# Performance work log

Measured on AMD Instinct MI355X. Metric: run time of the kernel, lower is better.

Reference implementation:

```python
import jax, jax.numpy as jnp
import numpy as np

B, N, CIN = 8, 16384, 256
G, K, C, H, L = 16, 128, 256, 8, 2


def setup_inputs() -> dict:
    key = jax.random.key(0)
    ks = jax.random.split(key, 8)
    f = lambda k, s: jax.random.normal(k, s, dtype=jnp.float32)
    return dict(
        x=f(ks[0], (B, N, CIN)),
        W_lin=f(ks[1], (CIN, C)) * 0.02,
        b_lin=jnp.zeros((C,), jnp.float32),
        emb=f(ks[2], (G, K, C)),  # learned_embedding ~ randn in torch
        in_proj_w=f(ks[3], (L, 3 * C, C)) * 0.02,
        in_proj_b=jnp.zeros((L, 3 * C), jnp.float32),
        out_w=f(ks[4], (L, C, C)) * 0.02,
        out_b=jnp.zeros((L, C), jnp.float32),
        lin_w=f(ks[5], (L, C, C)) * 0.02,
        lin_b=jnp.zeros((L, C), jnp.float32),
        ln1_w=jnp.ones((L, C), jnp.float32),
        ln1_b=jnp.zeros((L, C), jnp.float32),
        ln2_w=jnp.ones((L, C), jnp.float32),
        ln2_b=jnp.zeros((L, C), jnp.float32),
    )


def _layernorm(x, w, b, eps=1e-5):
    m = x.mean(-1, keepdims=True)
    v = jnp.var(x, axis=-1, keepdims=True)
    return (x - m) / jnp.sqrt(v + eps) * w + b


def reference(x, W_lin, b_lin, emb, in_proj_w, in_proj_b, out_w, out_b,
              lin_w, lin_b, ln1_w, ln1_b, ln2_w, ln2_b):
    B_, N_, Cin = x.shape
    T = N_ // G  # tokens per group
    # grouped projection: [B,G,T,C]
    x4 = x.reshape(B_, G, T, Cin) @ W_lin + b_lin
    # cross-attn scores [B,G,K,T]; softmax over the LATENT axis k (dim=-2)
    scores = jnp.einsum('gkd,bgtd->bgkt', emb, x4) * (1.0 / jnp.sqrt(jnp.float32(C)))
    attn = jax.nn.softmax(scores, axis=2)
    y = jnp.einsum('bgkt,bgtd->bgkd', attn, x4)  # [B,G,K,C]
    # torch MHA with batch_first=False: (B*G) is SEQUENCE, K is BATCH
    y = y.reshape(B_ * G, K, C)  # (S, Nb, C)
    S = B_ * G
    Dh = C // H
    scale = 1.0 / jnp.sqrt(jnp.float32(Dh))
    for i in range(L):
        qkv = y @ in_proj_w[i].T + in_proj_b[i]
        q, k, v = jnp.split(qkv, 3, axis=-1)
        q = q.reshape(S, K, H, Dh)
        k = k.reshape(S, K, H, Dh)
        v = v.reshape(S, K, H, Dh)
        s2 = jnp.einsum('snhd,tnhd->nhst', q, k) * scale  # (Nb,H,S,S)
        a = jax.nn.softmax(s2, axis=-1)
        o = jnp.einsum('nhst,tnhd->snhd', a, v).reshape(S, K, C)
        o = o @ out_w[i].T + out_b[i]
        y = _layernorm(o + y, ln1_w[i], ln1_b[i])
        y = _layernorm(y @ lin_w[i].T + lin_b[i] + y, ln2_w[i], ln2_b[i])
    out = y.reshape(B_, G * K, C)
    return (out, attn)
```

## Files before the change

kernel.cpp:

```cpp
#include <hip/hip_runtime.h>

typedef __attribute__((ext_vector_type(4))) float  f32x4;
typedef __attribute__((ext_vector_type(8))) short  s16x8;

static __device__ __forceinline__ short f2bf(float f) {
    unsigned int x = __builtin_bit_cast(unsigned int, f);
    x += 0x7fffu + ((x >> 16) & 1u);
    return (short)(x >> 16);
}

__global__ __launch_bounds__(256) void castk(const float* __restrict__ in,
                                             short* __restrict__ out, int n) {
    int i = blockIdx.x * 256 + threadIdx.x;
    if (i < n) out[i] = f2bf(in[i]);
}

__global__ __launch_bounds__(256) void tcast256(const float* __restrict__ in,
                                                short* __restrict__ out) {
    out[blockIdx.x * 256 + threadIdx.x] = f2bf(in[threadIdx.x * 256 + blockIdx.x]);
}

template<bool AF32, bool OF32, bool OB16>
__global__ __launch_bounds__(256) void gemm_bt(
    const void* __restrict__ Av, const short* __restrict__ Bm,
    const float* __restrict__ bias,
    float* __restrict__ Cf, short* __restrict__ Cb,
    int M, int N, int K)
{
    __shared__ short lsA[128 * 40];
    __shared__ short lsB[128 * 40];
    const int tid = threadIdx.x;
    const int m0 = blockIdx.x * 128;
    const int n0 = blockIdx.y * 128;
    const int lane = tid & 63;
    const int w = tid >> 6;
    const int wmi = w >> 1, wni = w & 1;
    const int lr = lane & 15, ko = lane >> 4;
    const int r0 = tid >> 1, oc0 = (tid * 2) & 3;

    f32x4 acc[4][4] = {};
    for (int k0 = 0; k0 < K; k0 += 32) {
        __syncthreads();
        if constexpr (AF32) {
            const float* Ap = (const float*)Av + (size_t)(m0 + r0) * K + k0 + oc0 * 8;
            f32x4 a0 = *(const f32x4*)(Ap);
            f32x4 a1 = *(const f32x4*)(Ap + 4);
            f32x4 a2 = *(const f32x4*)(Ap + 8);
            f32x4 a3 = *(const f32x4*)(Ap + 12);
            s16x8 w0, w1;
            #pragma unroll
            for (int j = 0; j < 4; ++j) {
                w0[j] = f2bf(a0[j]); w0[4 + j] = f2bf(a1[j]);
                w1[j] = f2bf(a2[j]); w1[4 + j] = f2bf(a3[j]);
            }
            *(s16x8*)&lsA[r0 * 40 + oc0 * 8]     = w0;
            *(s16x8*)&lsA[r0 * 40 + oc0 * 8 + 8] = w1;
        } else {
            const short* Ap = (const short*)Av + (size_t)(m0 + r0) * K + k0 + oc0 * 8;
            *(s16x8*)&lsA[r0 * 40 + oc0 * 8]     = *(const s16x8*)Ap;
            *(s16x8*)&lsA[r0 * 40 + oc0 * 8 + 8] = *(const s16x8*)(Ap + 8);
        }
        const short* Bp = Bm + (size_t)(n0 + r0) * K + k0 + oc0 * 8;
        *(s16x8*)&lsB[r0 * 40 + oc0 * 8]     = *(const s16x8*)Bp;
        *(s16x8*)&lsB[r0 * 40 + oc0 * 8 + 8] = *(const s16x8*)(Bp + 8);
        __syncthreads();
        #pragma unroll
        for (int mt = 0; mt < 4; ++mt) {
            s16x8 a = *(const s16x8*)&lsA[(wmi * 64 + mt * 16 + lr) * 40 + ko * 8];
            #pragma unroll
            for (int nt = 0; nt < 4; ++nt) {
                s16x8 b = *(const s16x8*)&lsB[(wni * 64 + nt * 16 + lr) * 40 + ko * 8];
                acc[mt][nt] = __builtin_amdgcn_mfma_f32_16x16x32_bf16(a, b, acc[mt][nt], 0, 0, 0);
            }
        }
    }
    const int cr = ko * 4, cc = lr;
    #pragma unroll
    for (int mt = 0; mt < 4; ++mt)
    #pragma unroll
    for (int nt = 0; nt < 4; ++nt) {
        const int col = n0 + wni * 64 + nt * 16 + cc;
        const float bv = bias ? bias[col] : 0.f;
        #pragma unroll
        for (int j = 0; j < 4; ++j) {
            const int row = m0 + wmi * 64 + mt * 16 + cr + j;
            float v = acc[mt][nt][j] + bv;
            size_t idx = (size_t)row * N + col;
            if constexpr (OF32) Cf[idx] = v;
            if constexpr (OB16) Cb[idx] = f2bf(v);
        }
    }
}

__global__ __launch_bounds__(256) void scores_softmax(
    const short* __restrict__ embb, const short* __restrict__ x4b,
    float* __restrict__ attnF, short* __restrict__ attnB)
{
    __shared__ short lsA[128 * 40];
    __shared__ short lsB[128 * 40];
    __shared__ float redm[2 * 128];
    __shared__ float reds[2 * 128];
    const int tid = threadIdx.x;
    const int z = blockIdx.y;
    const int g = z & 15;
    const int t0 = blockIdx.x * 128;
    const short* A = embb + (size_t)g * 32768;
    const short* B = x4b + (size_t)z * 262144 + (size_t)t0 * 256;
    const int lane = tid & 63;
    const int w = tid >> 6;
    const int wmi = w >> 1, wni = w & 1;
    const int lr = lane & 15, ko = lane >> 4;
    const int r0 = tid >> 1, oc0 = (tid * 2) & 3;

    f32x4 acc[4][4] = {};
    for (int k0 = 0; k0 < 256; k0 += 32) {
        __syncthreads();
        const short* Ap = A + (size_t)r0 * 256 + k0 + oc0 * 8;
        *(s16x8*)&lsA[r0 * 40 + oc0 * 8]     = *(const s16x8*)Ap;
        *(s16x8*)&lsA[r0 * 40 + oc0 * 8 + 8] = *(const s16x8*)(Ap + 8);
        const short* Bp = B + (size_t)r0 * 256 + k0 + oc0 * 8;
        *(s16x8*)&lsB[r0 * 40 + oc0 * 8]     = *(const s16x8*)Bp;
        *(s16x8*)&lsB[r0 * 40 + oc0 * 8 + 8] = *(const s16x8*)(Bp + 8);
        __syncthreads();
        #pragma unroll
        for (int mt = 0; mt < 4; ++mt) {
            s16x8 a = *(const s16x8*)&lsA[(wmi * 64 + mt * 16 + lr) * 40 + ko * 8];
            #pragma unroll
            for (int nt = 0; nt < 4; ++nt) {
                s16x8 b = *(const s16x8*)&lsB[(wni * 64 + nt * 16 + lr) * 40 + ko * 8];
                acc[mt][nt] = __builtin_amdgcn_mfma_f32_16x16x32_bf16(a, b, acc[mt][nt], 0, 0, 0);
            }
        }
    }
    const float scale = 0.0625f;
    float cm[4];
    #pragma unroll
    for (int nt = 0; nt < 4; ++nt) {
        float m = -1e30f;
        #pragma unroll
        for (int mt = 0; mt < 4; ++mt)
            #pragma unroll
            for (int j = 0; j < 4; ++j) m = fmaxf(m, acc[mt][nt][j]);
        m = fmaxf(m, __shfl_xor(m, 16));
        m = fmaxf(m, __shfl_xor(m, 32));
        cm[nt] = m * scale;
    }
    if (lane < 16) {
        #pragma unroll
        for (int nt = 0; nt < 4; ++nt)
            redm[wmi * 128 + wni * 64 + nt * 16 + lr] = cm[nt];
    }
    __syncthreads();
    float cmax[4];
    #pragma unroll
    for (int nt = 0; nt < 4; ++nt) {
        int c = wni * 64 + nt * 16 + lr;
        cmax[nt] = fmaxf(redm[c], redm[128 + c]);
    }
    float cs[4];
    #pragma unroll
    for (int nt = 0; nt < 4; ++nt) {
        float s = 0.f;
        #pragma unroll
        for (int mt = 0; mt < 4; ++mt)
            #pragma unroll
            for (int j = 0; j < 4; ++j) {
                float p = __expf(acc[mt][nt][j] * scale - cmax[nt]);
                acc[mt][nt][j] = p;
                s += p;
            }
        s += __shfl_xor(s, 16);
        s += __shfl_xor(s, 32);
        cs[nt] = s;
    }
    if (lane < 16) {
        #pragma unroll
        for (int nt = 0; nt < 4; ++nt)
            reds[wmi * 128 + wni * 64 + nt * 16 + lr] = cs[nt];
    }
    __syncthreads();
    #pragma unroll
    for (int nt = 0; nt < 4; ++nt) {
        int c = wni * 64 + nt * 16 + lr;
        float inv = 1.f / (reds[c] + reds[128 + c]);
        int col = t0 + c;
        #pragma unroll
        for (int mt = 0; mt < 4; ++mt)
            #pragma unroll
            for (int j = 0; j < 4; ++j) {
                int row = wmi * 64 + mt * 16 + ko * 4 + j;
                float a = acc[mt][nt][j] * inv;
                size_t idx = ((size_t)(z * 128 + row)) * 1024 + col;
                attnF[idx] = a;
                attnB[idx] = f2bf(a);
            }
    }
}

__global__ __launch_bounds__(256) void y_gemm(
    const short* __restrict__ attnB, const short* __restrict__ x4b,
    float* __restrict__ yF, short* __restrict__ yB)
{
    __shared__ short lsA[128 * 40];
    __shared__ short lsB[128 * 40];
    const int tid = threadIdx.x;
    const int z = blockIdx.y;
    const int d0 = blockIdx.x * 128;
    const short* A = attnB + (size_t)z * 131072;
    const short* X = x4b + (size_t)z * 262144 + d0;
    const int lane = tid & 63;
    const int w = tid >> 6;
    const int wmi = w >> 1, wni = w & 1;
    const int lr = lane & 15, ko = lane >> 4;
    const int r0 = tid >> 1, oc0 = (tid * 2) & 3;
    const int rb = tid >> 3, ocb = (tid * 2) & 15;
    f32x4 acc[4][4] = {};
    for (int k0 = 0; k0 < 1024; k0 += 32) {
        __syncthreads();
        const short* Ap = A + (size_t)r0 * 1024 + k0 + oc0 * 8;
        *(s16x8*)&lsA[r0 * 40 + oc0 * 8]     = *(const s16x8*)Ap;
        *(s16x8*)&lsA[r0 * 40 + oc0 * 8 + 8] = *(const s16x8*)(Ap + 8);
        s16x8 v0 = *(const s16x8*)(X + (size_t)(k0 + rb) * 256 + ocb * 8);
        s16x8 v1 = *(const s16x8*)(X + (size_t)(k0 + rb) * 256 + ocb * 8 + 8);
        #pragma unroll
        for (int j = 0; j < 8; ++j) {
            int dd = ocb * 8 + j;
            lsB[dd * 40 + ((((rb >> 3) ^ ((dd >> 4) & 3)) << 3) | (rb & 7))] = v0[j];
            int dd2 = dd + 8;
            lsB[dd2 * 40 + ((((rb >> 3) ^ ((dd2 >> 4) & 3)) << 3) | (rb & 7))] = v1[j];
        }
        __syncthreads();
        #pragma unroll
        for (int mt = 0; mt < 4; ++mt) {
            s16x8 a = *(const s16x8*)&lsA[(wmi * 64 + mt * 16 + lr) * 40 + ko * 8];
            #pragma unroll
            for (int nt = 0; nt < 4; ++nt) {
                int dd = wni * 64 + nt * 16 + lr;
                s16x8 b = *(const s16x8*)&lsB[dd * 40 + ((ko ^ ((dd >> 4) & 3)) << 3)];
                acc[mt][nt] = __builtin_amdgcn_mfma_f32_16x16x32_bf16(a, b, acc[mt][nt], 0, 0, 0);
            }
        }
    }
    const int cr = ko * 4, cc = lr;
    #pragma unroll
    for (int mt = 0; mt < 4; ++mt)
    #pragma unroll
    for (int nt = 0; nt < 4; ++nt)
        #pragma unroll
        for (int j = 0; j < 4; ++j) {
            int krow = wmi * 64 + mt * 16 + cr + j;
            int col = d0 + wni * 64 + nt * 16 + cc;
            float v = acc[mt][nt][j];
            size_t idx = ((size_t)(z * 128 + krow)) * 256 + col;
            yF[idx] = v;
            yB[idx] = f2bf(v);
        }
}

__global__ __launch_bounds__(256) void mha(
    const short* __restrict__ qkvb, short* __restrict__ ob)
{
    __shared__ short la[128 * 136];
    __shared__ short lvt[32 * 136];
    __shared__ float redm[2 * 128];
    __shared__ float reds[2 * 128];
    short* lq = la;
    short* lk = la + 128 * 40;
    const int tid = threadIdx.x;
    const int nb = blockIdx.x >> 3;
    const int h = blockIdx.x & 7;
    const int lane = tid & 63;
    const int w = tid >> 6;
    const int wmi = w >> 1, wni = w & 1;
    const int lr = lane & 15, ko = lane >> 4;
    const int sv = tid >> 1, oc0 = (tid * 2) & 3;
    {
        const short* qp = qkvb + ((size_t)sv * 128 + nb) * 768 + h * 32 + oc0 * 8;
        *(s16x8*)&lq[sv * 40 + oc0 * 8]     = *(const s16x8*)qp;
        *(s16x8*)&lq[sv * 40 + oc0 * 8 + 8] = *(const s16x8*)(qp + 8);
        const short* kp = qp + 256;
        *(s16x8*)&lk[sv * 40 + oc0 * 8]     = *(const s16x8*)kp;
        *(s16x8*)&lk[sv * 40 + oc0 * 8 + 8] = *(const s16x8*)(kp + 8);
        const short* vp = qp + 512;
        s16x8 v0 = *(const s16x8*)vp;
        s16x8 v1 = *(const s16x8*)(vp + 8);
        #pragma unroll
        for (int j = 0; j < 8; ++j) {
            lvt[(oc0 * 8 + j) * 136 + sv]     = v0[j];
            lvt[(oc0 * 8 + 8 + j) * 136 + sv] = v1[j];
        }
    }
    __syncthreads();
    f32x4 acc[4][4] = {};
    #pragma unroll
    for (int mt = 0; mt < 4; ++mt) {
        s16x8 a = *(const s16x8*)&lq[(wmi * 64 + mt * 16 + lr) * 40 + ko * 8];
        #pragma unroll
        for (int nt = 0; nt < 4; ++nt) {
            s16x8 b = *(const s16x8*)&lk[(wni * 64 + nt * 16 + lr) * 40 + ko * 8];
            acc[mt][nt] = __builtin_amdgcn_mfma_f32_16x16x32_bf16(a, b, acc[mt][nt], 0, 0, 0);
        }
    }
    const float scale = 0.1767766953f;
    float rm[4][4];
    #pragma unroll
    for (int mt = 0; mt < 4; ++mt)
        #pragma unroll
        for (int j = 0; j < 4; ++j) {
            float m = -1e30f;
            #pragma unroll
            for (int nt = 0; nt < 4; ++nt) m = fmaxf(m, acc[mt][nt][j]);
            m = fmaxf(m, __shfl_xor(m, 1));
            m = fmaxf(m, __shfl_xor(m, 2));
            m = fmaxf(m, __shfl_xor(m, 4));
            m = fmaxf(m, __shfl_xor(m, 8));
            rm[mt][j] = m * scale;
        }
    if (lr == 0) {
        #pragma unroll
        for (int mt = 0; mt < 4; ++mt)
            #pragma unroll
            for (int j = 0; j < 4; ++j)
                redm[wni * 128 + wmi * 64 + mt * 16 + ko * 4 + j] = rm[mt][j];
    }
    __syncthreads();
    float rs[4][4];
    #pragma unroll
    for (int mt = 0; mt < 4; ++mt)
        #pragma unroll
        for (int j = 0; j < 4; ++j) {
            int row = wmi * 64 + mt * 16 + ko * 4 + j;
            float mx = fmaxf(redm[row], redm[128 + row]);
            float s = 0.f;
            #pragma unroll
            for (int nt = 0; nt < 4; ++nt) {
                float p = __expf(acc[mt][nt][j] * scale - mx);
                acc[mt][nt][j] = p;
                s += p;
            }
            s += __shfl_xor(s, 1);
            s += __shfl_xor(s, 2);
            s += __shfl_xor(s, 4);
            s += __shfl_xor(s, 8);
            rs[mt][j] = s;
        }
    if (lr == 0) {
        #pragma unroll
        for (int mt = 0; mt < 4; ++mt)
            #pragma unroll
            for (int j = 0; j < 4; ++j)
                reds[wni * 128 + wmi * 64 + mt * 16 + ko * 4 + j] = rs[mt][j];
    }
    __syncthreads();
    #pragma unroll
    for (int mt = 0; mt < 4; ++mt)
        #pragma unroll
        for (int j = 0; j < 4; ++j) {
            int row = wmi * 64 + mt * 16 + ko * 4 + j;
            float inv = 1.f / (reds[row] + reds[128 + row]);
            #pragma unroll
            for (int nt = 0; nt < 4; ++nt) {
                int col = wni * 64 + nt * 16 + lr;
                la[row * 136 + col] = f2bf(acc[mt][nt][j] * inv);
            }
        }
    __syncthreads();
    f32x4 acc2[2][2] = {};
    #pragma unroll
    for (int ks = 0; ks < 4; ++ks)
        #pragma unroll
        for (int mt = 0; mt < 2; ++mt) {
            s16x8 a = *(const s16x8*)&la[(w * 32 + mt * 16 + lr) * 136 + ks * 32 + ko * 8];
            #pragma unroll
            for (int nt = 0; nt < 2; ++nt) {
                s16x8 b = *(const s16x8*)&lvt[(nt * 16 + lr) * 136 + ks * 32 + ko * 8];
                acc2[mt][nt] = __builtin_amdgcn_mfma_f32_16x16x32_bf16(a, b, acc2[mt][nt], 0, 0, 0);
            }
        }
    const int cr = ko * 4, cc = lr;
    #pragma unroll
    for (int mt = 0; mt < 2; ++mt)
    #pragma unroll
    for (int nt = 0; nt < 2; ++nt)
        #pragma unroll
        for (int j = 0; j < 4; ++j) {
            int s = w * 32 + mt * 16 + cr + j;
            int d = nt * 16 + cc;
            ob[((size_t)s * 128 + nb) * 256 + h * 32 + d] = f2bf(acc2[mt][nt][j]);
        }
}

__global__ __launch_bounds__(256) void ln_res(
    const float* __restrict__ zin, const float* __restrict__ res,
    const float* __restrict__ gw, const float* __restrict__ gb,
    float* __restrict__ outF, short* __restrict__ outB)
{
    const int row = blockIdx.x;
    const int t = threadIdx.x;
    const size_t idx = (size_t)row * 256 + t;
    float v = zin[idx] + res[idx];
    float s1 = v, s2 = v * v;
    #pragma unroll
    for (int o = 1; o < 64; o <<= 1) {
        s1 += __shfl_xor(s1, o);
        s2 += __shfl_xor(s2, o);
    }
    __shared__ float ps[8];
    const int wv = t >> 6;
    if ((t & 63) == 0) { ps[wv] = s1; ps[4 + wv] = s2; }
    __syncthreads();
    float S1 = ps[0] + ps[1] + ps[2] + ps[3];
    float S2 = ps[4] + ps[5] + ps[6] + ps[7];
    float m = S1 * 0.00390625f;
    float var = S2 * 0.00390625f - m * m;
    float rstd = rsqrtf(var + 1e-5f);
    float o = (v - m) * rstd * gw[t] + gb[t];
    outF[idx] = o;
    outB[idx] = f2bf(o);
}

extern "C" void kernel_launch(void* const* d_in, const int* in_sizes, int n_in,
                              void* d_out, int out_size, void* d_ws, size_t ws_size,
                              hipStream_t stream)
{
    const float* x    = (const float*)d_in[0];
    const float* Wlin = (const float*)d_in[1];
    const float* blin = (const float*)d_in[2];
    const float* emb  = (const float*)d_in[3];
    const float* ipw  = (const float*)d_in[4];
    const float* ipb  = (const float*)d_in[5];
    const float* outw = (const float*)d_in[6];
    const float* outb = (const float*)d_in[7];
    const float* linw = (const float*)d_in[8];
    const float* linb = (const float*)d_in[9];
    const float* ln1w = (const float*)d_in[10];
    const float* ln1b = (const float*)d_in[11];
    const float* ln2w = (const float*)d_in[12];
    const float* ln2b = (const float*)d_in[13];

    char* ws = (char*)d_ws;
    short* x4_b   = (short*)(ws);
    short* attn_b = (short*)(ws + 67108864);
    float* yF     = (float*)(ws + 100663296);
    short* y_b    = (short*)(ws + 117440512);
    char*  wb     = ws + 125829120;
    short* WT_b   = (short*)(wb);
    short* emb_b  = (short*)(wb + 131072);
    short* inw_b  = (short*)(wb + 131072 + 1048576);
    short* outw_b = (short*)(wb + 131072 + 1048576 + 786432);
    short* linw_b = (short*)(wb + 131072 + 1048576 + 786432 + 262144);
    short* qkv_b  = (short*)(ws);
    short* o_b    = (short*)(ws + 25165824);
    float* op     = (float*)(ws + 33554432);

    float* out_y    = (float*)d_out;
    float* out_attn = (float*)d_out + 4194304;

    castk<<<dim3(2048), dim3(256), 0, stream>>>(emb, emb_b, 524288);
    castk<<<dim3(1536), dim3(256), 0, stream>>>(ipw, inw_b, 393216);
    castk<<<dim3(512),  dim3(256), 0, stream>>>(outw, outw_b, 131072);
    castk<<<dim3(512),  dim3(256), 0, stream>>>(linw, linw_b, 131072);
    tcast256<<<dim3(256), dim3(256), 0, stream>>>(Wlin, WT_b);

    gemm_bt<true, false, true><<<dim3(1024, 2), dim3(256), 0, stream>>>(
        x, WT_b, blin, nullptr, x4_b, 131072, 256, 256);
    scores_softmax<<<dim3(8, 128), dim3(256), 0, stream>>>(emb_b, x4_b, out_attn, attn_b);
    y_gemm<<<dim3(2, 128), dim3(256), 0, stream>>>(attn_b, x4_b, yF, y_b);

    for (int i = 0; i < 2; ++i) {
        gemm_bt<false, false, true><<<dim3(128, 6), dim3(256), 0, stream>>>(
            y_b, inw_b + i * 196608, ipb + i * 768, nullptr, qkv_b, 16384, 768, 256);
        mha<<<dim3(1024), dim3(256), 0, stream>>>(qkv_b, o_b);
        gemm_bt<false, true, false><<<dim3(128, 2), dim3(256), 0, stream>>>(
            o_b, outw_b + i * 65536, outb + i * 256, op, nullptr, 16384, 256, 256);
        ln_res<<<dim3(16384), dim3(256), 0, stream>>>(
            op, yF, ln1w + i * 256, ln1b + i * 256, yF, y_b);
        gemm_bt<false, true, false><<<dim3(128, 2), dim3(256), 0, stream>>>(
            y_b, linw_b + i * 65536, linb + i * 256, op, nullptr, 16384, 256, 256);
        ln_res<<<dim3(16384), dim3(256), 0, stream>>>(
            op, yF, ln2w + i * 256, ln2b + i * 256, (i == 1) ? out_y : yF, y_b);
    }
}
```

Before: 561.9 us.

## Prefetch next K-tile into registers in GEMM kernels and merge weight casts

The GEMM-style kernels (gemm_bt, scores_softmax, y_gemm) now issue the global loads for the next K-slice into registers before running the MFMA loop on the current LDS tile. This lets global memory latency overlap with compute instead of stalling at the top of each iteration. The four separate weight-cast launches are merged into one vectorized castall kernel, which cuts launch overhead. The prefetch adds register pressure, and the barrier count per iteration stays at two.

```diff
diff --git a/kernel.cpp b/kernel.cpp
--- a/kernel.cpp
+++ b/kernel.cpp
@@ -2,6 +2,7 @@
 
 typedef __attribute__((ext_vector_type(4))) float  f32x4;
 typedef __attribute__((ext_vector_type(8))) short  s16x8;
+typedef __attribute__((ext_vector_type(4))) short  s16x4;
 
 static __device__ __forceinline__ short f2bf(float f) {
     unsigned int x = __builtin_bit_cast(unsigned int, f);
@@ -9,10 +10,23 @@
     return (short)(x >> 16);
 }
 
-__global__ __launch_bounds__(256) void castk(const float* __restrict__ in,
-                                             short* __restrict__ out, int n) {
-    int i = blockIdx.x * 256 + threadIdx.x;
-    if (i < n) out[i] = f2bf(in[i]);
+__global__ __launch_bounds__(256) void castall(
+    const float* __restrict__ emb, const float* __restrict__ ipw,
+    const float* __restrict__ outw, const float* __restrict__ linw,
+    short* __restrict__ de, short* __restrict__ di,
+    short* __restrict__ dg, short* __restrict__ dl)
+{
+    int q = blockIdx.x * 256 + threadIdx.x;
+    const float* s; short* d; int o;
+    if (q < 131072)      { s = emb;  d = de; o = q; }
+    else if (q < 229376) { s = ipw;  d = di; o = q - 131072; }
+    else if (q < 262144) { s = outw; d = dg; o = q - 229376; }
+    else                 { s = linw; d = dl; o = q - 262144; }
+    f32x4 v = *(const f32x4*)(s + (size_t)o * 4);
+    s16x4 r;
+    #pragma unroll
+    for (int j = 0; j < 4; ++j) r[j] = f2bf(v[j]);
+    *(s16x4*)(d + (size_t)o * 4) = r;
 }
 
 __global__ __launch_bounds__(256) void tcast256(const float* __restrict__ in,
@@ -38,32 +52,56 @@
     const int lr = lane & 15, ko = lane >> 4;
     const int r0 = tid >> 1, oc0 = (tid * 2) & 3;
 
+    const float* Apf = (const float*)Av + (size_t)(m0 + r0) * K + oc0 * 8;
+    const short* Aps = (const short*)Av + (size_t)(m0 + r0) * K + oc0 * 8;
+    const short* Bp  = Bm + (size_t)(n0 + r0) * K + oc0 * 8;
+
+    f32x4 pa0, pa1, pa2, pa3;
+    s16x8 pas0, pas1, pb0, pb1;
+    if constexpr (AF32) {
+        pa0 = *(const f32x4*)(Apf);
+        pa1 = *(const f32x4*)(Apf + 4);
+        pa2 = *(const f32x4*)(Apf + 8);
+        pa3 = *(const f32x4*)(Apf + 12);
+    } else {
+        pas0 = *(const s16x8*)(Aps);
+        pas1 = *(const s16x8*)(Aps + 8);
+    }
+    pb0 = *(const s16x8*)(Bp);
+    pb1 = *(const s16x8*)(Bp + 8);
+
     f32x4 acc[4][4] = {};
     for (int k0 = 0; k0 < K; k0 += 32) {
-        __syncthreads();
         if constexpr (AF32) {
-            const float* Ap = (const float*)Av + (size_t)(m0 + r0) * K + k0 + oc0 * 8;
-            f32x4 a0 = *(const f32x4*)(Ap);
-            f32x4 a1 = *(const f32x4*)(Ap + 4);
-            f32x4 a2 = *(const f32x4*)(Ap + 8);
-            f32x4 a3 = *(const f32x4*)(Ap + 12);
             s16x8 w0, w1;
             #pragma unroll
             for (int j = 0; j < 4; ++j) {
-                w0[j] = f2bf(a0[j]); w0[4 + j] = f2bf(a1[j]);
-                w1[j] = f2bf(a2[j]); w1[4 + j] = f2bf(a3[j]);
+                w0[j] = f2bf(pa0[j]); w0[4 + j] = f2bf(pa1[j]);
+                w1[j] = f2bf(pa2[j]); w1[4 + j] = f2bf(pa3[j]);
             }
             *(s16x8*)&lsA[r0 * 40 + oc0 * 8]     = w0;
             *(s16x8*)&lsA[r0 * 40 + oc0 * 8 + 8] = w1;
         } else {
-            const short* Ap = (const short*)Av + (size_t)(m0 + r0) * K + k0 + oc0 * 8;
-            *(s16x8*)&lsA[r0 * 40 + oc0 * 8]     = *(const s16x8*)Ap;
-            *(s16x8*)&lsA[r0 * 40 + oc0 * 8 + 8] = *(const s16x8*)(Ap + 8);
-        }
-        const short* Bp = Bm + (size_t)(n0 + r0) * K + k0 + oc0 * 8;
-        *(s16x8*)&lsB[r0 * 40 + oc0 * 8]     = *(const s16x8*)Bp;
-        *(s16x8*)&lsB[r0 * 40 + oc0 * 8 + 8] = *(const s16x8*)(Bp + 8);
+            *(s16x8*)&lsA[r0 * 40 + oc0 * 8]     = pas0;
+            *(s16x8*)&lsA[r0 * 40 + oc0 * 8 + 8] = pas1;
+        }
+        *(s16x8*)&lsB[r0 * 40 + oc0 * 8]     = pb0;
+        *(s16x8*)&lsB[r0 * 40 + oc0 * 8 + 8] = pb1;
         __syncthreads();
+        if (k0 + 32 < K) {
+            const int kn = k0 + 32;
+            if constexpr (AF32) {
+                pa0 = *(const f32x4*)(Apf + kn);
+                pa1 = *(const f32x4*)(Apf + kn + 4);
+                pa2 = *(const f32x4*)(Apf + kn + 8);
+                pa3 = *(const f32x4*)(Apf + kn + 12);
+            } else {
+                pas0 = *(const s16x8*)(Aps + kn);
+                pas1 = *(const s16x8*)(Aps + kn + 8);
+            }
+            pb0 = *(const s16x8*)(Bp + kn);
+            pb1 = *(const s16x8*)(Bp + kn + 8);
+        }
         #pragma unroll
         for (int mt = 0; mt < 4; ++mt) {
             s16x8 a = *(const s16x8*)&lsA[(wmi * 64 + mt * 16 + lr) * 40 + ko * 8];
@@ -73,6 +111,7 @@
                 acc[mt][nt] = __builtin_amdgcn_mfma_f32_16x16x32_bf16(a, b, acc[mt][nt], 0, 0, 0);
             }
         }
+        __syncthreads();
     }
     const int cr = ko * 4, cc = lr;
     #pragma unroll
@@ -112,16 +151,27 @@
     const int lr = lane & 15, ko = lane >> 4;
     const int r0 = tid >> 1, oc0 = (tid * 2) & 3;
 
+    const short* Ap = A + (size_t)r0 * 256 + oc0 * 8;
+    const short* Bp = B + (size_t)r0 * 256 + oc0 * 8;
+    s16x8 pa0 = *(const s16x8*)(Ap);
+    s16x8 pa1 = *(const s16x8*)(Ap + 8);
+    s16x8 pb0 = *(const s16x8*)(Bp);
+    s16x8 pb1 = *(const s16x8*)(Bp + 8);
+
     f32x4 acc[4][4] = {};
     for (int k0 = 0; k0 < 256; k0 += 32) {
+        *(s16x8*)&lsA[r0 * 40 + oc0 * 8]     = pa0;
+        *(s16x8*)&lsA[r0 * 40 + oc0 * 8 + 8] = pa1;
+        *(s16x8*)&lsB[r0 * 40 + oc0 * 8]     = pb0;
+        *(s16x8*)&lsB[r0 * 40 + oc0 * 8 + 8] = pb1;
         __syncthreads();
-        const short* Ap = A + (size_t)r0 * 256 + k0 + oc0 * 8;
-        *(s16x8*)&lsA[r0 * 40 + oc0 * 8]     = *(const s16x8*)Ap;
-        *(s16x8*)&lsA[r0 * 40 + oc0 * 8 + 8] = *(const s16x8*)(Ap + 8);
-        const short* Bp = B + (size_t)r0 * 256 + k0 + oc0 * 8;
-        *(s16x8*)&lsB[r0 * 40 + oc0 * 8]     = *(const s16x8*)Bp;
-        *(s16x8*)&lsB[r0 * 40 + oc0 * 8 + 8] = *(const s16x8*)(Bp + 8);
-        __syncthreads();
+        if (k0 + 32 < 256) {
+            const int kn = k0 + 32;
+            pa0 = *(const s16x8*)(Ap + kn);
+            pa1 = *(const s16x8*)(Ap + kn + 8);
+            pb0 = *(const s16x8*)(Bp + kn);
+            pb1 = *(const s16x8*)(Bp + kn + 8);
+        }
         #pragma unroll
         for (int mt = 0; mt < 4; ++mt) {
             s16x8 a = *(const s16x8*)&lsA[(wmi * 64 + mt * 16 + lr) * 40 + ko * 8];
@@ -131,6 +181,7 @@
                 acc[mt][nt] = __builtin_amdgcn_mfma_f32_16x16x32_bf16(a, b, acc[mt][nt], 0, 0, 0);
             }
         }
+        __syncthreads();
     }
     const float scale = 0.0625f;
     float cm[4];
@@ -214,22 +265,33 @@
     const int lr = lane & 15, ko = lane >> 4;
     const int r0 = tid >> 1, oc0 = (tid * 2) & 3;
     const int rb = tid >> 3, ocb = (tid * 2) & 15;
+
+    const short* Ap = A + (size_t)r0 * 1024 + oc0 * 8;
+    const short* Xp = X + (size_t)rb * 256 + ocb * 8;
+
+    s16x8 pa0 = *(const s16x8*)(Ap);
+    s16x8 pa1 = *(const s16x8*)(Ap + 8);
+    s16x8 pv0 = *(const s16x8*)(Xp);
+    s16x8 pv1 = *(const s16x8*)(Xp + 8);
+
     f32x4 acc[4][4] = {};
     for (int k0 = 0; k0 < 1024; k0 += 32) {
-        __syncthreads();
-        const short* Ap = A + (size_t)r0 * 1024 + k0 + oc0 * 8;
-        *(s16x8*)&lsA[r0 * 40 + oc0 * 8]     = *(const s16x8*)Ap;
-        *(s16x8*)&lsA[r0 * 40 + oc0 * 8 + 8] = *(const s16x8*)(Ap + 8);
-        s16x8 v0 = *(const s16x8*)(X + (size_t)(k0 + rb) * 256 + ocb * 8);
-        s16x8 v1 = *(const s16x8*)(X + (size_t)(k0 + rb) * 256 + ocb * 8 + 8);
+        *(s16x8*)&lsA[r0 * 40 + oc0 * 8]     = pa0;
+        *(s16x8*)&lsA[r0 * 40 + oc0 * 8 + 8] = pa1;
         #pragma unroll
         for (int j = 0; j < 8; ++j) {
             int dd = ocb * 8 + j;
-            lsB[dd * 40 + ((((rb >> 3) ^ ((dd >> 4) & 3)) << 3) | (rb & 7))] = v0[j];
+            lsB[dd * 40 + ((((rb >> 3) ^ ((dd >> 4) & 3)) << 3) | (rb & 7))] = pv0[j];
             int dd2 = dd + 8;
-            lsB[dd2 * 40 + ((((rb >> 3) ^ ((dd2 >> 4) & 3)) << 3) | (rb & 7))] = v1[j];
+            lsB[dd2 * 40 + ((((rb >> 3) ^ ((dd2 >> 4) & 3)) << 3) | (rb & 7))] = pv1[j];
         }
         __syncthreads();
+        if (k0 + 32 < 1024) {
+            pa0 = *(const s16x8*)(Ap + k0 + 32);
+            pa1 = *(const s16x8*)(Ap + k0 + 40);
+            pv0 = *(const s16x8*)(Xp + (size_t)(k0 + 32) * 256);
+            pv1 = *(const s16x8*)(Xp + (size_t)(k0 + 32) * 256 + 8);
+        }
         #pragma unroll
         for (int mt = 0; mt < 4; ++mt) {
             s16x8 a = *(const s16x8*)&lsA[(wmi * 64 + mt * 16 + lr) * 40 + ko * 8];
@@ -240,6 +302,7 @@
                 acc[mt][nt] = __builtin_amdgcn_mfma_f32_16x16x32_bf16(a, b, acc[mt][nt], 0, 0, 0);
             }
         }
+        __syncthreads();
     }
     const int cr = ko * 4, cc = lr;
     #pragma unroll
@@ -456,10 +519,8 @@
     float* out_y    = (float*)d_out;
     float* out_attn = (float*)d_out + 4194304;
 
-    castk<<<dim3(2048), dim3(256), 0, stream>>>(emb, emb_b, 524288);
-    castk<<<dim3(1536), dim3(256), 0, stream>>>(ipw, inw_b, 393216);
-    castk<<<dim3(512),  dim3(256), 0, stream>>>(outw, outw_b, 131072);
-    castk<<<dim3(512),  dim3(256), 0, stream>>>(linw, linw_b, 131072);
+    castall<<<dim3(1152), dim3(256), 0, stream>>>(emb, ipw, outw, linw,
+                                                  emb_b, inw_b, outw_b, linw_b);
     tcast256<<<dim3(256), dim3(256), 0, stream>>>(Wlin, WT_b);
 
     gemm_bt<true, false, true><<<dim3(1024, 2), dim3(256), 0, stream>>>(
```

Result: faster. 540.9 us (-3.7%).
